# Optimization experiments

Measured on AMD Instinct MI355X. Metric: run time of the kernel, lower is better.

## Reference

```python
import jax, jax.numpy as jnp
import numpy as np

N = 100000
E = 3200000
F_IN = 16
H = 128
LAT = 64
L = 3
G = 1024


def setup_inputs() -> dict:
    key = jax.random.key(0)
    ks = jax.random.split(key, 12)
    x = jax.random.normal(ks[0], (N, F_IN), dtype=jnp.float32)
    edge_index = jax.random.randint(ks[1], (2, E), 0, N, dtype=jnp.int64)
    batch = jnp.sort(jax.random.randint(ks[2], (N,), 0, G, dtype=jnp.int64))
    batch = batch.at[-1].set(G - 1)  # ensure batch.max()+1 == G
    s_in = 1.0 / np.sqrt(F_IN)
    s_h = 1.0 / np.sqrt(H)
    W_in = jax.random.uniform(ks[3], (F_IN, H), jnp.float32, -s_in, s_in)
    b_in = jax.random.uniform(ks[4], (H,), jnp.float32, -s_in, s_in)
    W_msg = jax.random.uniform(ks[5], (L, H, H), jnp.float32, -s_h, s_h)
    b_msg = jax.random.uniform(ks[6], (L, H), jnp.float32, -s_h, s_h)
    W_mean = jax.random.uniform(ks[7], (H, LAT), jnp.float32, -s_h, s_h)
    b_mean = jax.random.uniform(ks[8], (LAT,), jnp.float32, -s_h, s_h)
    W_logvar = jax.random.uniform(ks[9], (H, LAT), jnp.float32, -s_h, s_h)
    b_logvar = jax.random.uniform(ks[10], (LAT,), jnp.float32, -s_h, s_h)
    return {
        "x": x, "edge_index": edge_index, "batch": batch, "num_graphs": G,
        "W_in": W_in, "b_in": b_in, "W_msg": W_msg, "b_msg": b_msg,
        "W_mean": W_mean, "b_mean": b_mean,
        "W_logvar": W_logvar, "b_logvar": b_logvar,
    }


def reference(x, edge_index, batch, num_graphs, W_in, b_in, W_msg, b_msg,
              W_mean, b_mean, W_logvar, b_logvar):
    src, dst = edge_index[0], edge_index[1]
    n = x.shape[0]
    # input net: Linear + ReLU
    h = jax.nn.relu(x @ W_in + b_in)  # [N, H]
    # stacked message-passing: transform, gather at src, scatter-add to dst, ReLU
    for l in range(L):
        m = h @ W_msg[l] + b_msg[l]                    # [N, H]
        agg = jax.ops.segment_sum(m[src], dst, num_segments=n)  # [N, H]
        h = jax.nn.relu(agg)
    # graph-level sum pooling via index_add over batch ids
    graph_embedding = jax.ops.segment_sum(h, batch, num_segments=num_graphs)  # [G, H]
    z_mean = graph_embedding @ W_mean + b_mean
    z_logvar = graph_embedding @ W_logvar + b_logvar
    return (z_mean, z_logvar)
```

## Files before the change

kernel.cpp:

```cpp
#include <hip/hip_runtime.h>

constexpr int N_  = 100000;
constexpr int E_  = 3200000;
constexpr int FIN = 16;
constexpr int H_  = 128;
constexpr int LAT = 64;
constexpr int L_  = 3;
constexpr int G_  = 1024;

constexpr int BSH = 9;
constexpr int BNODES = 1 << BSH;
constexpr int NB_ = (N_ + BNODES - 1) / BNODES;
constexpr int FILL_NB = 512;
constexpr int FILL_CHUNK = E_ / FILL_NB;

using bf16x8 = __attribute__((ext_vector_type(8))) short;
using f32x4  = __attribute__((ext_vector_type(4))) float;

__device__ inline float bflo(unsigned int u) {
  union { unsigned int i; float f; } v; v.i = u << 16; return v.f;
}
__device__ inline float bfhi(unsigned int u) {
  union { unsigned int i; float f; } v; v.i = u & 0xffff0000u; return v.f;
}
__device__ inline unsigned short f2bf(float f) {
  union { float f; unsigned int i; } v; v.f = f;
  unsigned int r = v.i + 0x7fffu + ((v.i >> 16) & 1u);
  return (unsigned short)(r >> 16);
}

__global__ __launch_bounds__(256) void k_wconv(const float* __restrict__ W,
                                               unsigned short* __restrict__ Wt,
                                               int* __restrict__ bcnt) {
  if (blockIdx.x == 0) {
    for (int i = threadIdx.x; i < NB_; i += 256) bcnt[i] = 0;
  }
  const int idx = blockIdx.x * 256 + threadIdx.x;
  if (idx < L_ * H_ * H_) {
    const int l = idx >> 14, rem = idx & 16383;
    const int c = rem >> 7, k = rem & 127;
    Wt[idx] = f2bf(W[l * H_ * H_ + k * H_ + c]);
  }
}

__global__ __launch_bounds__(256) void k_input(const float* __restrict__ x,
                                               const float* __restrict__ Win,
                                               const float* __restrict__ bin,
                                               unsigned short* __restrict__ h) {
  __shared__ float Wl[FIN * H_];
  __shared__ float xl[4 * FIN];
  const int tid = threadIdx.x;
  for (int i = tid; i < FIN * H_; i += 256) Wl[i] = Win[i];
  const int n0 = blockIdx.x * 4;
  if (tid < 4 * FIN) xl[tid] = x[(size_t)n0 * FIN + tid];
  __syncthreads();
  const int nl = tid >> 6, l = tid & 63;
  float a0 = bin[2 * l], a1 = bin[2 * l + 1];
#pragma unroll
  for (int k = 0; k < FIN; ++k) {
    const float xv = xl[nl * FIN + k];
    a0 += xv * Wl[k * H_ + 2 * l];
    a1 += xv * Wl[k * H_ + 2 * l + 1];
  }
  const unsigned int packed =
      (unsigned int)f2bf(fmaxf(a0, 0.f)) | ((unsigned int)f2bf(fmaxf(a1, 0.f)) << 16);
  *reinterpret_cast<unsigned int*>(h + (size_t)(n0 + nl) * H_ + 2 * l) = packed;
}

__global__ __launch_bounds__(256) void k_msg_mfma(const unsigned short* __restrict__ h,
                                                  const unsigned short* __restrict__ Wt,
                                                  const float* __restrict__ b,
                                                  unsigned short* __restrict__ m) {
  __shared__ unsigned short st[4][32][40];
  const int wave = threadIdx.x >> 6;
  const int lane = threadIdx.x & 63;
  const int r = lane & 15;
  const int g = lane >> 4;
  const int n0 = blockIdx.x * 32;
  const int cb = wave * 32;

  f32x4 acc[2][2] = {};
#pragma unroll
  for (int kk = 0; kk < 4; ++kk) {
    const int koff = kk * 32 + g * 8;
    const bf16x8 a0 = *reinterpret_cast<const bf16x8*>(h + (size_t)(n0 + r) * H_ + koff);
    const bf16x8 a1 = *reinterpret_cast<const bf16x8*>(h + (size_t)(n0 + 16 + r) * H_ + koff);
    const bf16x8 b0 = *reinterpret_cast<const bf16x8*>(Wt + (size_t)(cb + r) * H_ + koff);
    const bf16x8 b1 = *reinterpret_cast<const bf16x8*>(Wt + (size_t)(cb + 16 + r) * H_ + koff);
    acc[0][0] = __builtin_amdgcn_mfma_f32_16x16x32_bf16(a0, b0, acc[0][0], 0, 0, 0);
    acc[0][1] = __builtin_amdgcn_mfma_f32_16x16x32_bf16(a0, b1, acc[0][1], 0, 0, 0);
    acc[1][0] = __builtin_amdgcn_mfma_f32_16x16x32_bf16(a1, b0, acc[1][0], 0, 0, 0);
    acc[1][1] = __builtin_amdgcn_mfma_f32_16x16x32_bf16(a1, b1, acc[1][1], 0, 0, 0);
  }

  const float bc0 = b[cb + r];
  const float bc1 = b[cb + 16 + r];
#pragma unroll
  for (int rt = 0; rt < 2; ++rt)
#pragma unroll
    for (int ct = 0; ct < 2; ++ct) {
      const float bc = ct ? bc1 : bc0;
#pragma unroll
      for (int j = 0; j < 4; ++j)
        st[wave][rt * 16 + g * 4 + j][ct * 16 + r] = f2bf(acc[rt][ct][j] + bc);
    }
  __syncthreads();
#pragma unroll
  for (int p = 0; p < 2; ++p) {
    const int lr = p * 16 + (lane >> 2);
    const int seg = lane & 3;
    const bf16x8 v = *reinterpret_cast<const bf16x8*>(&st[wave][lr][seg * 8]);
    *reinterpret_cast<bf16x8*>(m + (size_t)(n0 + lr) * H_ + cb + seg * 8) = v;
  }
}

__global__ __launch_bounds__(256) void k_bhist(const int* __restrict__ ei,
                                               int* __restrict__ bcnt) {
  __shared__ int lh[NB_];
  for (int i = threadIdx.x; i < NB_; i += 256) lh[i] = 0;
  __syncthreads();
  const int gid = blockIdx.x * 256 + threadIdx.x;
  const int stride = gridDim.x * 256;
  for (int e = gid; e < E_; e += stride) atomicAdd(&lh[ei[E_ + e] >> BSH], 1);
  __syncthreads();
  for (int i = threadIdx.x; i < NB_; i += 256)
    if (lh[i]) atomicAdd(&bcnt[i], lh[i]);
}

__global__ __launch_bounds__(256) void k_bscan(const int* __restrict__ bcnt,
                                               int* __restrict__ boff,
                                               int* __restrict__ bcur,
                                               float* __restrict__ ge) {
  __shared__ int s[256];
  const int t = threadIdx.x;
  s[t] = (t < NB_) ? bcnt[t] : 0;
  __syncthreads();
  for (int off = 1; off < 256; off <<= 1) {
    const int add = (t >= off) ? s[t - off] : 0;
    __syncthreads();
    s[t] += add;
    __syncthreads();
  }
  const int ex = (t == 0) ? 0 : s[t - 1];
  if (t < NB_) { boff[t] = ex; bcur[t] = ex; }
  if (t == 0) boff[NB_] = s[NB_ - 1];
  float4 z = make_float4(0.f, 0.f, 0.f, 0.f);
  float4* g4 = reinterpret_cast<float4*>(ge);
  for (int i = t; i < G_ * H_ / 4; i += 256) g4[i] = z;
}

__global__ __launch_bounds__(256) void k_bfill(const int* __restrict__ ei,
                                               int* __restrict__ bcur,
                                               unsigned int* __restrict__ ebuf) {
  __shared__ int lh[NB_], lbase[NB_];
  const int t = threadIdx.x;
  for (int i = t; i < NB_; i += 256) lh[i] = 0;
  __syncthreads();
  const int e0 = blockIdx.x * FILL_CHUNK;
  const int e1 = e0 + FILL_CHUNK;
  for (int e = e0 + t; e < e1; e += 256) atomicAdd(&lh[ei[E_ + e] >> BSH], 1);
  __syncthreads();
  for (int i = t; i < NB_; i += 256) {
    const int c = lh[i];
    lbase[i] = c ? atomicAdd(&bcur[i], c) : 0;
  }
  __syncthreads();
  for (int i = t; i < NB_; i += 256) lh[i] = 0;
  __syncthreads();
  for (int e = e0 + t; e < e1; e += 256) {
    const int src = ei[e], dst = ei[E_ + e];
    const int b = dst >> BSH;
    const int pos = lbase[b] + atomicAdd(&lh[b], 1);
    ebuf[pos] = ((unsigned)src << BSH) | (unsigned)(dst & (BNODES - 1));
  }
}

__global__ __launch_bounds__(256) void k_bcsr(const unsigned int* __restrict__ ebuf,
                                              const int* __restrict__ boff,
                                              int* __restrict__ rowp,
                                              int* __restrict__ ssrc) {
  __shared__ int sdeg[BNODES];
  __shared__ int scur[BNODES];
  __shared__ int part[256];
  const int b = blockIdx.x;
  const int nbase = b << BSH;
  const int ncnt = min(BNODES, N_ - nbase);
  const int ebeg = boff[b], eend = boff[b + 1];
  const int t = threadIdx.x;
  for (int i = t; i < BNODES; i += 256) { sdeg[i] = 0; scur[i] = 0; }
  __syncthreads();
  for (int e = ebeg + t; e < eend; e += 256)
    atomicAdd(&sdeg[ebuf[e] & (BNODES - 1)], 1);
  __syncthreads();
  const int i0 = 2 * t, i1 = 2 * t + 1;
  const int d0 = sdeg[i0];
  part[t] = d0 + sdeg[i1];
  __syncthreads();
  for (int off = 1; off < 256; off <<= 1) {
    const int add = (t >= off) ? part[t - off] : 0;
    __syncthreads();
    part[t] += add;
    __syncthreads();
  }
  const int ex = (t == 0) ? 0 : part[t - 1];
  sdeg[i0] = ex;
  sdeg[i1] = ex + d0;
  __syncthreads();
  for (int i = t; i < ncnt; i += 256) rowp[nbase + i] = ebeg + sdeg[i];
  if (b == NB_ - 1 && t == 0) rowp[N_] = E_;
  for (int e = ebeg + t; e < eend; e += 256) {
    const unsigned int ed = ebuf[e];
    const int ld = ed & (BNODES - 1);
    const int pos = ebeg + sdeg[ld] + atomicAdd(&scur[ld], 1);
    ssrc[pos] = (int)(ed >> BSH);
  }
}

__global__ __launch_bounds__(256) void k_gather(const unsigned short* __restrict__ m,
                                                const int* __restrict__ rowptr,
                                                const int* __restrict__ ssrc,
                                                unsigned short* __restrict__ h) {
  const int n = blockIdx.x * 4 + (threadIdx.x >> 6);
  const int c2 = threadIdx.x & 63;
  const int beg = rowptr[n], end = rowptr[n + 1];
  const unsigned short* mc = m + 2 * c2;
  float a0 = 0.f, a1 = 0.f;
  int i = beg;
  for (; i + 15 < end; i += 16) {
    int s[16];
#pragma unroll
    for (int u = 0; u < 16; ++u) s[u] = ssrc[i + u];
    unsigned int v[16];
#pragma unroll
    for (int u = 0; u < 16; ++u)
      v[u] = *reinterpret_cast<const unsigned int*>(mc + (size_t)s[u] * H_);
#pragma unroll
    for (int u = 0; u < 16; ++u) { a0 += bflo(v[u]); a1 += bfhi(v[u]); }
  }
  for (; i + 3 < end; i += 4) {
    int s[4];
#pragma unroll
    for (int u = 0; u < 4; ++u) s[u] = ssrc[i + u];
    unsigned int v[4];
#pragma unroll
    for (int u = 0; u < 4; ++u)
      v[u] = *reinterpret_cast<const unsigned int*>(mc + (size_t)s[u] * H_);
#pragma unroll
    for (int u = 0; u < 4; ++u) { a0 += bflo(v[u]); a1 += bfhi(v[u]); }
  }
  for (; i < end; ++i) {
    const unsigned int v = *reinterpret_cast<const unsigned int*>(mc + (size_t)ssrc[i] * H_);
    a0 += bflo(v);  a1 += bfhi(v);
  }
  const unsigned int packed =
      (unsigned int)f2bf(fmaxf(a0, 0.f)) | ((unsigned int)f2bf(fmaxf(a1, 0.f)) << 16);
  *reinterpret_cast<unsigned int*>(h + (size_t)n * H_ + 2 * c2) = packed;
}

constexpr int POOL_CHUNK = 128;
__global__ __launch_bounds__(128) void k_pool(const unsigned short* __restrict__ h,
                                              const int* __restrict__ batch,
                                              float* __restrict__ ge) {
  __shared__ int bl[POOL_CHUNK];
  const int tid = threadIdx.x;
  const int start = blockIdx.x * POOL_CHUNK;
  const int cnt = min(POOL_CHUNK, N_ - start);
  if (tid < cnt) bl[tid] = batch[start + tid];
  __syncthreads();
  float run = 0.f;
  int cur = bl[0];
  for (int i = 0; i < cnt; ++i) {
    const int bid = bl[i];
    const float v = bflo((unsigned int)h[(size_t)(start + i) * H_ + tid]);
    if (bid != cur) {
      unsafeAtomicAdd(&ge[(size_t)cur * H_ + tid], run);
      run = 0.f;
      cur = bid;
    }
    run += v;
  }
  unsafeAtomicAdd(&ge[(size_t)cur * H_ + tid], run);
}

__global__ __launch_bounds__(128) void k_out(const float* __restrict__ ge,
                                             const float* __restrict__ Wm,
                                             const float* __restrict__ bm,
                                             const float* __restrict__ Wv,
                                             const float* __restrict__ bv,
                                             float* __restrict__ out) {
  __shared__ float gl[H_];
  const int g = blockIdx.x, tid = threadIdx.x;
  gl[tid] = ge[(size_t)g * H_ + tid];
  __syncthreads();
  const bool is_mean = (tid < LAT);
  const float* W = is_mean ? Wm : Wv;
  const float* bb = is_mean ? bm : bv;
  const int c = tid & 63;
  float acc = bb[c];
#pragma unroll 8
  for (int k = 0; k < H_; ++k) acc += gl[k] * W[k * LAT + c];
  const size_t off = is_mean ? 0 : (size_t)G_ * LAT;
  out[off + (size_t)g * LAT + c] = acc;
}

extern "C" void kernel_launch(void* const* d_in, const int* in_sizes, int n_in,
                              void* d_out, int out_size, void* d_ws, size_t ws_size,
                              hipStream_t stream) {
  const float* x     = (const float*)d_in[0];
  const int*   ei    = (const int*)d_in[1];
  const int*   batch = (const int*)d_in[2];
  const float* Win   = (const float*)d_in[4];
  const float* bin   = (const float*)d_in[5];
  const float* Wmsg  = (const float*)d_in[6];
  const float* bmsg  = (const float*)d_in[7];
  const float* Wmean = (const float*)d_in[8];
  const float* bmean = (const float*)d_in[9];
  const float* Wlv   = (const float*)d_in[10];
  const float* blv   = (const float*)d_in[11];
  float* out = (float*)d_out;

  char* p = (char*)d_ws;
  unsigned short* h  = (unsigned short*)p;  p += (size_t)N_ * H_ * 2;
  unsigned short* m  = (unsigned short*)p;  p += (size_t)N_ * H_ * 2;
  unsigned int* ebuf = (unsigned int*)p;    p += (size_t)E_ * 4;
  int* ssrc          = (int*)p;             p += (size_t)E_ * 4;
  int* rowp          = (int*)p;             p += (size_t)(N_ + 1) * 4;
  unsigned short* Wt = (unsigned short*)p;  p += (size_t)L_ * H_ * H_ * 2;
  float* ge          = (float*)p;           p += (size_t)G_ * H_ * 4;
  int* bcnt          = (int*)p;             p += (size_t)NB_ * 4;
  int* boff          = (int*)p;             p += (size_t)(NB_ + 1) * 4;
  int* bcur          = (int*)p;             p += (size_t)NB_ * 4;

  k_wconv<<<(L_ * H_ * H_ + 255) / 256, 256, 0, stream>>>(Wmsg, Wt, bcnt);

  k_bhist<<<256, 256, 0, stream>>>(ei, bcnt);
  k_bscan<<<1, 256, 0, stream>>>(bcnt, boff, bcur, ge);
  k_bfill<<<FILL_NB, 256, 0, stream>>>(ei, bcur, ebuf);
  k_bcsr<<<NB_, 256, 0, stream>>>(ebuf, boff, rowp, ssrc);

  k_input<<<N_ / 4, 256, 0, stream>>>(x, Win, bin, h);

  for (int l = 0; l < L_; ++l) {
    k_msg_mfma<<<N_ / 32, 256, 0, stream>>>(h, Wt + (size_t)l * H_ * H_,
                                            bmsg + (size_t)l * H_, m);
    k_gather<<<N_ / 4, 256, 0, stream>>>(m, rowp, ssrc, h);
  }

  k_pool<<<(N_ + POOL_CHUNK - 1) / POOL_CHUNK, 128, 0, stream>>>(h, batch, ge);

  k_out<<<G_, 128, 0, stream>>>(ge, Wmean, bmean, Wlv, blv, out);
}
```

Baseline: 559.3 us.

## Fuse gather with next layer's MFMA transform and merge weight-convert with input layer

Adds a k_gm kernel that gathers and sums neighbour messages for 32 nodes into shared memory, applies ReLU, then runs the next layer's bf16 MFMA transform directly. This removes the h write and re-read between the gather and the message kernels for layers two and three. The weight conversion and the input Linear+ReLU are merged into one launch, and the bucket-histogram grid is doubled. The fused gather runs only 256 threads per 32 nodes, so it has less parallelism for latency hiding, and it needs a second message buffer.

```diff
diff --git a/kernel.cpp b/kernel.cpp
--- a/kernel.cpp
+++ b/kernel.cpp
@@ -14,6 +14,8 @@
 constexpr int FILL_NB = 512;
 constexpr int FILL_CHUNK = E_ / FILL_NB;
 
+constexpr int WCONV_BLOCKS = (L_ * H_ * H_) / 256;
+
 using bf16x8 = __attribute__((ext_vector_type(8))) short;
 using f32x4  = __attribute__((ext_vector_type(4))) float;
 
@@ -29,29 +31,27 @@
   return (unsigned short)(r >> 16);
 }
 
-__global__ __launch_bounds__(256) void k_wconv(const float* __restrict__ W,
+__global__ __launch_bounds__(256) void k_winit(const float* __restrict__ W,
                                                unsigned short* __restrict__ Wt,
-                                               int* __restrict__ bcnt) {
-  if (blockIdx.x == 0) {
-    for (int i = threadIdx.x; i < NB_; i += 256) bcnt[i] = 0;
-  }
-  const int idx = blockIdx.x * 256 + threadIdx.x;
-  if (idx < L_ * H_ * H_) {
+                                               int* __restrict__ bcnt,
+                                               const float* __restrict__ x,
+                                               const float* __restrict__ Win,
+                                               const float* __restrict__ bin,
+                                               unsigned short* __restrict__ h) {
+  const int tid = threadIdx.x;
+  if (blockIdx.x < WCONV_BLOCKS) {
+    if (blockIdx.x == 0)
+      for (int i = tid; i < NB_; i += 256) bcnt[i] = 0;
+    const int idx = blockIdx.x * 256 + tid;
     const int l = idx >> 14, rem = idx & 16383;
     const int c = rem >> 7, k = rem & 127;
     Wt[idx] = f2bf(W[l * H_ * H_ + k * H_ + c]);
-  }
-}
-
-__global__ __launch_bounds__(256) void k_input(const float* __restrict__ x,
-                                               const float* __restrict__ Win,
-                                               const float* __restrict__ bin,
-                                               unsigned short* __restrict__ h) {
+    return;
+  }
   __shared__ float Wl[FIN * H_];
   __shared__ float xl[4 * FIN];
-  const int tid = threadIdx.x;
   for (int i = tid; i < FIN * H_; i += 256) Wl[i] = Win[i];
-  const int n0 = blockIdx.x * 4;
+  const int n0 = (blockIdx.x - WCONV_BLOCKS) * 4;
   if (tid < 4 * FIN) xl[tid] = x[(size_t)n0 * FIN + tid];
   __syncthreads();
   const int nl = tid >> 6, l = tid & 63;
@@ -111,6 +111,95 @@
     const int seg = lane & 3;
     const bf16x8 v = *reinterpret_cast<const bf16x8*>(&st[wave][lr][seg * 8]);
     *reinterpret_cast<bf16x8*>(m + (size_t)(n0 + lr) * H_ + cb + seg * 8) = v;
+  }
+}
+
+__global__ __launch_bounds__(256) void k_gm(const unsigned short* __restrict__ m_in,
+                                            const int* __restrict__ rowptr,
+                                            const int* __restrict__ ssrc,
+                                            const unsigned short* __restrict__ Wt,
+                                            const float* __restrict__ b,
+                                            unsigned short* __restrict__ m_out) {
+  __shared__ unsigned int hl[32][68];
+  __shared__ unsigned short st[4][32][40];
+  const int wave = threadIdx.x >> 6;
+  const int lane = threadIdx.x & 63;
+  const int n0 = blockIdx.x * 32;
+  const unsigned short* mc = m_in + 2 * lane;
+
+  for (int j = 0; j < 8; ++j) {
+    const int row = wave * 8 + j;
+    const int n = n0 + row;
+    const int beg = rowptr[n], end = rowptr[n + 1];
+    float a0 = 0.f, a1 = 0.f;
+    int i = beg;
+    for (; i + 15 < end; i += 16) {
+      int s[16];
+#pragma unroll
+      for (int u = 0; u < 16; ++u) s[u] = ssrc[i + u];
+      unsigned int v[16];
+#pragma unroll
+      for (int u = 0; u < 16; ++u)
+        v[u] = *reinterpret_cast<const unsigned int*>(mc + (size_t)s[u] * H_);
+#pragma unroll
+      for (int u = 0; u < 16; ++u) { a0 += bflo(v[u]); a1 += bfhi(v[u]); }
+    }
+    for (; i + 3 < end; i += 4) {
+      int s[4];
+#pragma unroll
+      for (int u = 0; u < 4; ++u) s[u] = ssrc[i + u];
+      unsigned int v[4];
+#pragma unroll
+      for (int u = 0; u < 4; ++u)
+        v[u] = *reinterpret_cast<const unsigned int*>(mc + (size_t)s[u] * H_);
+#pragma unroll
+      for (int u = 0; u < 4; ++u) { a0 += bflo(v[u]); a1 += bfhi(v[u]); }
+    }
+    for (; i < end; ++i) {
+      const unsigned int v = *reinterpret_cast<const unsigned int*>(mc + (size_t)ssrc[i] * H_);
+      a0 += bflo(v);  a1 += bfhi(v);
+    }
+    hl[row][lane] =
+        (unsigned int)f2bf(fmaxf(a0, 0.f)) | ((unsigned int)f2bf(fmaxf(a1, 0.f)) << 16);
+  }
+  __syncthreads();
+
+  const int r = lane & 15;
+  const int g = lane >> 4;
+  const int cb = wave * 32;
+  f32x4 acc[2][2] = {};
+#pragma unroll
+  for (int kk = 0; kk < 4; ++kk) {
+    const int koff  = kk * 32 + g * 8;
+    const int koffu = kk * 16 + g * 4;
+    const bf16x8 a0 = *reinterpret_cast<const bf16x8*>(&hl[r][koffu]);
+    const bf16x8 a1 = *reinterpret_cast<const bf16x8*>(&hl[16 + r][koffu]);
+    const bf16x8 b0 = *reinterpret_cast<const bf16x8*>(Wt + (size_t)(cb + r) * H_ + koff);
+    const bf16x8 b1 = *reinterpret_cast<const bf16x8*>(Wt + (size_t)(cb + 16 + r) * H_ + koff);
+    acc[0][0] = __builtin_amdgcn_mfma_f32_16x16x32_bf16(a0, b0, acc[0][0], 0, 0, 0);
+    acc[0][1] = __builtin_amdgcn_mfma_f32_16x16x32_bf16(a0, b1, acc[0][1], 0, 0, 0);
+    acc[1][0] = __builtin_amdgcn_mfma_f32_16x16x32_bf16(a1, b0, acc[1][0], 0, 0, 0);
+    acc[1][1] = __builtin_amdgcn_mfma_f32_16x16x32_bf16(a1, b1, acc[1][1], 0, 0, 0);
+  }
+
+  const float bc0 = b[cb + r];
+  const float bc1 = b[cb + 16 + r];
+#pragma unroll
+  for (int rt = 0; rt < 2; ++rt)
+#pragma unroll
+    for (int ct = 0; ct < 2; ++ct) {
+      const float bc = ct ? bc1 : bc0;
+#pragma unroll
+      for (int j = 0; j < 4; ++j)
+        st[wave][rt * 16 + g * 4 + j][ct * 16 + r] = f2bf(acc[rt][ct][j] + bc);
+    }
+  __syncthreads();
+#pragma unroll
+  for (int p = 0; p < 2; ++p) {
+    const int lr = p * 16 + (lane >> 2);
+    const int seg = lane & 3;
+    const bf16x8 v = *reinterpret_cast<const bf16x8*>(&st[wave][lr][seg * 8]);
+    *reinterpret_cast<bf16x8*>(m_out + (size_t)(n0 + lr) * H_ + cb + seg * 8) = v;
   }
 }
 
@@ -321,7 +410,8 @@
 
   char* p = (char*)d_ws;
   unsigned short* h  = (unsigned short*)p;  p += (size_t)N_ * H_ * 2;
-  unsigned short* m  = (unsigned short*)p;  p += (size_t)N_ * H_ * 2;
+  unsigned short* mA = (unsigned short*)p;  p += (size_t)N_ * H_ * 2;
+  unsigned short* mB = (unsigned short*)p;  p += (size_t)N_ * H_ * 2;
   unsigned int* ebuf = (unsigned int*)p;    p += (size_t)E_ * 4;
   int* ssrc          = (int*)p;             p += (size_t)E_ * 4;
   int* rowp          = (int*)p;             p += (size_t)(N_ + 1) * 4;
@@ -331,22 +421,20 @@
   int* boff          = (int*)p;             p += (size_t)(NB_ + 1) * 4;
   int* bcur          = (int*)p;             p += (size_t)NB_ * 4;
 
-  k_wconv<<<(L_ * H_ * H_ + 255) / 256, 256, 0, stream>>>(Wmsg, Wt, bcnt);
-
-  k_bhist<<<256, 256, 0, stream>>>(ei, bcnt);
+  k_winit<<<WCONV_BLOCKS + N_ / 4, 256, 0, stream>>>(Wmsg, Wt, bcnt, x, Win, bin, h);
+
+  k_bhist<<<512, 256, 0, stream>>>(ei, bcnt);
   k_bscan<<<1, 256, 0, stream>>>(bcnt, boff, bcur, ge);
   k_bfill<<<FILL_NB, 256, 0, stream>>>(ei, bcur, ebuf);
   k_bcsr<<<NB_, 256, 0, stream>>>(ebuf, boff, rowp, ssrc);
 
-  k_input<<<N_ / 4, 256, 0, stream>>>(x, Win, bin, h);
-
-  for (int l = 0; l < L_; ++l) {
-    k_msg_mfma<<<N_ / 32, 256, 0, stream>>>(h, Wt + (size_t)l * H_ * H_,
-                                            bmsg + (size_t)l * H_, m);
-    k_gather<<<N_ / 4, 256, 0, stream>>>(m, rowp, ssrc, h);
-  }
+  k_msg_mfma<<<N_ / 32, 256, 0, stream>>>(h, Wt, bmsg, mA);
+  k_gm<<<N_ / 32, 256, 0, stream>>>(mA, rowp, ssrc,
+                                    Wt + (size_t)H_ * H_, bmsg + H_, mB);
+  k_gm<<<N_ / 32, 256, 0, stream>>>(mB, rowp, ssrc,
+                                    Wt + (size_t)2 * H_ * H_, bmsg + 2 * H_, mA);
+  k_gather<<<N_ / 4, 256, 0, stream>>>(mA, rowp, ssrc, h);
 
   k_pool<<<(N_ + POOL_CHUNK - 1) / POOL_CHUNK, 128, 0, stream>>>(h, batch, ge);
-
   k_out<<<G_, 128, 0, stream>>>(ge, Wmean, bmean, Wlv, blv, out);
 }
```

After: 559.0 us. Within noise of the previous version (-0.1%).

## Chunk message features into 16-column slabs and gather per chunk with wave-split edges

Applied to the files above, without the earlier changes.

Stores messages and hidden states in a chunked layout of 8 slabs of 16 bf16 columns (N×16 each), so each gather block works on one 32-byte column slab whose 3.2 MB working set is more likely to stay in cache during random source reads. The gather kernel now spreads a node's edges across 16 lane groups with a shuffle reduction, and uses a fixed grid of persistent slots. Weight conversion and the input layer are merged into one launch, and the histogram grid is doubled. In exchange, each node's edge list and row pointers are read eight times, once per slab, and the pool kernel reads with a 32-byte stride.

```diff
diff --git a/kernel.cpp b/kernel.cpp
--- a/kernel.cpp
+++ b/kernel.cpp
@@ -14,6 +14,9 @@
 constexpr int FILL_NB = 512;
 constexpr int FILL_CHUNK = E_ / FILL_NB;
 
+constexpr int WCONV_BLOCKS = (L_ * H_ * H_) / 256;
+constexpr int GSLOTS = 4096;
+
 using bf16x8 = __attribute__((ext_vector_type(8))) short;
 using f32x4  = __attribute__((ext_vector_type(4))) float;
 
@@ -29,29 +32,27 @@
   return (unsigned short)(r >> 16);
 }
 
-__global__ __launch_bounds__(256) void k_wconv(const float* __restrict__ W,
+__global__ __launch_bounds__(256) void k_winit(const float* __restrict__ W,
                                                unsigned short* __restrict__ Wt,
-                                               int* __restrict__ bcnt) {
-  if (blockIdx.x == 0) {
-    for (int i = threadIdx.x; i < NB_; i += 256) bcnt[i] = 0;
-  }
-  const int idx = blockIdx.x * 256 + threadIdx.x;
-  if (idx < L_ * H_ * H_) {
+                                               int* __restrict__ bcnt,
+                                               const float* __restrict__ x,
+                                               const float* __restrict__ Win,
+                                               const float* __restrict__ bin,
+                                               unsigned short* __restrict__ h) {
+  const int tid = threadIdx.x;
+  if (blockIdx.x < WCONV_BLOCKS) {
+    if (blockIdx.x == 0)
+      for (int i = tid; i < NB_; i += 256) bcnt[i] = 0;
+    const int idx = blockIdx.x * 256 + tid;
     const int l = idx >> 14, rem = idx & 16383;
     const int c = rem >> 7, k = rem & 127;
     Wt[idx] = f2bf(W[l * H_ * H_ + k * H_ + c]);
-  }
-}
-
-__global__ __launch_bounds__(256) void k_input(const float* __restrict__ x,
-                                               const float* __restrict__ Win,
-                                               const float* __restrict__ bin,
-                                               unsigned short* __restrict__ h) {
+    return;
+  }
   __shared__ float Wl[FIN * H_];
   __shared__ float xl[4 * FIN];
-  const int tid = threadIdx.x;
   for (int i = tid; i < FIN * H_; i += 256) Wl[i] = Win[i];
-  const int n0 = blockIdx.x * 4;
+  const int n0 = (blockIdx.x - WCONV_BLOCKS) * 4;
   if (tid < 4 * FIN) xl[tid] = x[(size_t)n0 * FIN + tid];
   __syncthreads();
   const int nl = tid >> 6, l = tid & 63;
@@ -67,10 +68,11 @@
   *reinterpret_cast<unsigned int*>(h + (size_t)(n0 + nl) * H_ + 2 * l) = packed;
 }
 
-__global__ __launch_bounds__(256) void k_msg_mfma(const unsigned short* __restrict__ h,
+template <int CHUNKED>
+__global__ __launch_bounds__(256) void k_msg_mfma(const unsigned short* __restrict__ A,
                                                   const unsigned short* __restrict__ Wt,
                                                   const float* __restrict__ b,
-                                                  unsigned short* __restrict__ m) {
+                                                  unsigned short* __restrict__ m8) {
   __shared__ unsigned short st[4][32][40];
   const int wave = threadIdx.x >> 6;
   const int lane = threadIdx.x & 63;
@@ -83,8 +85,15 @@
 #pragma unroll
   for (int kk = 0; kk < 4; ++kk) {
     const int koff = kk * 32 + g * 8;
-    const bf16x8 a0 = *reinterpret_cast<const bf16x8*>(h + (size_t)(n0 + r) * H_ + koff);
-    const bf16x8 a1 = *reinterpret_cast<const bf16x8*>(h + (size_t)(n0 + 16 + r) * H_ + koff);
+    bf16x8 a0, a1;
+    if (CHUNKED) {
+      const size_t cbase = (size_t)(2 * kk + (g >> 1)) * N_ * 16 + (g & 1) * 8;
+      a0 = *reinterpret_cast<const bf16x8*>(A + cbase + (size_t)(n0 + r) * 16);
+      a1 = *reinterpret_cast<const bf16x8*>(A + cbase + (size_t)(n0 + 16 + r) * 16);
+    } else {
+      a0 = *reinterpret_cast<const bf16x8*>(A + (size_t)(n0 + r) * H_ + koff);
+      a1 = *reinterpret_cast<const bf16x8*>(A + (size_t)(n0 + 16 + r) * H_ + koff);
+    }
     const bf16x8 b0 = *reinterpret_cast<const bf16x8*>(Wt + (size_t)(cb + r) * H_ + koff);
     const bf16x8 b1 = *reinterpret_cast<const bf16x8*>(Wt + (size_t)(cb + 16 + r) * H_ + koff);
     acc[0][0] = __builtin_amdgcn_mfma_f32_16x16x32_bf16(a0, b0, acc[0][0], 0, 0, 0);
@@ -110,7 +119,8 @@
     const int lr = p * 16 + (lane >> 2);
     const int seg = lane & 3;
     const bf16x8 v = *reinterpret_cast<const bf16x8*>(&st[wave][lr][seg * 8]);
-    *reinterpret_cast<bf16x8*>(m + (size_t)(n0 + lr) * H_ + cb + seg * 8) = v;
+    *reinterpret_cast<bf16x8*>(m8 + (size_t)(2 * wave + (seg >> 1)) * N_ * 16 +
+                               (size_t)(n0 + lr) * 16 + (seg & 1) * 8) = v;
   }
 }
 
@@ -216,49 +226,54 @@
   }
 }
 
-__global__ __launch_bounds__(256) void k_gather(const unsigned short* __restrict__ m,
-                                                const int* __restrict__ rowptr,
-                                                const int* __restrict__ ssrc,
-                                                unsigned short* __restrict__ h) {
-  const int n = blockIdx.x * 4 + (threadIdx.x >> 6);
-  const int c2 = threadIdx.x & 63;
-  const int beg = rowptr[n], end = rowptr[n + 1];
-  const unsigned short* mc = m + 2 * c2;
-  float a0 = 0.f, a1 = 0.f;
-  int i = beg;
-  for (; i + 15 < end; i += 16) {
-    int s[16];
-#pragma unroll
-    for (int u = 0; u < 16; ++u) s[u] = ssrc[i + u];
-    unsigned int v[16];
-#pragma unroll
-    for (int u = 0; u < 16; ++u)
-      v[u] = *reinterpret_cast<const unsigned int*>(mc + (size_t)s[u] * H_);
-#pragma unroll
-    for (int u = 0; u < 16; ++u) { a0 += bflo(v[u]); a1 += bfhi(v[u]); }
-  }
-  for (; i + 3 < end; i += 4) {
-    int s[4];
-#pragma unroll
-    for (int u = 0; u < 4; ++u) s[u] = ssrc[i + u];
-    unsigned int v[4];
-#pragma unroll
-    for (int u = 0; u < 4; ++u)
-      v[u] = *reinterpret_cast<const unsigned int*>(mc + (size_t)s[u] * H_);
-#pragma unroll
-    for (int u = 0; u < 4; ++u) { a0 += bflo(v[u]); a1 += bfhi(v[u]); }
-  }
-  for (; i < end; ++i) {
-    const unsigned int v = *reinterpret_cast<const unsigned int*>(mc + (size_t)ssrc[i] * H_);
-    a0 += bflo(v);  a1 += bfhi(v);
-  }
-  const unsigned int packed =
-      (unsigned int)f2bf(fmaxf(a0, 0.f)) | ((unsigned int)f2bf(fmaxf(a1, 0.f)) << 16);
-  *reinterpret_cast<unsigned int*>(h + (size_t)n * H_ + 2 * c2) = packed;
+__global__ __launch_bounds__(256) void k_gather8(const unsigned short* __restrict__ m8,
+                                                 const int* __restrict__ rowptr,
+                                                 const int* __restrict__ ssrc,
+                                                 unsigned short* __restrict__ h8) {
+  const int chunk = blockIdx.x & 7;
+  const int lane = threadIdx.x & 63;
+  const int wave = threadIdx.x >> 6;
+  const int slot = (blockIdx.x >> 3) * 4 + wave;
+  const int eg = lane >> 2;
+  const int cl = lane & 3;
+  const unsigned short* mc = m8 + (size_t)chunk * N_ * 16 + cl * 4;
+  unsigned short* hc = h8 + (size_t)chunk * N_ * 16;
+
+  for (int n = slot; n < N_; n += GSLOTS) {
+    const int beg = rowptr[n], end = rowptr[n + 1];
+    float a0 = 0.f, a1 = 0.f, a2 = 0.f, a3 = 0.f;
+    int i = beg + eg;
+    for (; i + 16 < end; i += 32) {
+      const int s0 = ssrc[i];
+      const int s1 = ssrc[i + 16];
+      const uint2 v0 = *reinterpret_cast<const uint2*>(mc + (size_t)s0 * 16);
+      const uint2 v1 = *reinterpret_cast<const uint2*>(mc + (size_t)s1 * 16);
+      a0 += bflo(v0.x);  a1 += bfhi(v0.x);  a2 += bflo(v0.y);  a3 += bfhi(v0.y);
+      a0 += bflo(v1.x);  a1 += bfhi(v1.x);  a2 += bflo(v1.y);  a3 += bfhi(v1.y);
+    }
+    if (i < end) {
+      const int s = ssrc[i];
+      const uint2 v = *reinterpret_cast<const uint2*>(mc + (size_t)s * 16);
+      a0 += bflo(v.x);  a1 += bfhi(v.x);  a2 += bflo(v.y);  a3 += bfhi(v.y);
+    }
+#pragma unroll
+    for (int mask = 4; mask <= 32; mask <<= 1) {
+      a0 += __shfl_xor(a0, mask);
+      a1 += __shfl_xor(a1, mask);
+      a2 += __shfl_xor(a2, mask);
+      a3 += __shfl_xor(a3, mask);
+    }
+    if (lane < 4) {
+      uint2 o;
+      o.x = (unsigned int)f2bf(fmaxf(a0, 0.f)) | ((unsigned int)f2bf(fmaxf(a1, 0.f)) << 16);
+      o.y = (unsigned int)f2bf(fmaxf(a2, 0.f)) | ((unsigned int)f2bf(fmaxf(a3, 0.f)) << 16);
+      *reinterpret_cast<uint2*>(hc + (size_t)n * 16 + cl * 4) = o;
+    }
+  }
 }
 
 constexpr int POOL_CHUNK = 128;
-__global__ __launch_bounds__(128) void k_pool(const unsigned short* __restrict__ h,
+__global__ __launch_bounds__(128) void k_pool(const unsigned short* __restrict__ h8,
                                               const int* __restrict__ batch,
                                               float* __restrict__ ge) {
   __shared__ int bl[POOL_CHUNK];
@@ -267,11 +282,12 @@
   const int cnt = min(POOL_CHUNK, N_ - start);
   if (tid < cnt) bl[tid] = batch[start + tid];
   __syncthreads();
+  const unsigned short* hc = h8 + (size_t)(tid >> 4) * N_ * 16 + (tid & 15);
   float run = 0.f;
   int cur = bl[0];
   for (int i = 0; i < cnt; ++i) {
     const int bid = bl[i];
-    const float v = bflo((unsigned int)h[(size_t)(start + i) * H_ + tid]);
+    const float v = bflo((unsigned int)hc[(size_t)(start + i) * 16]);
     if (bid != cur) {
       unsafeAtomicAdd(&ge[(size_t)cur * H_ + tid], run);
       run = 0.f;
@@ -321,7 +337,8 @@
 
   char* p = (char*)d_ws;
   unsigned short* h  = (unsigned short*)p;  p += (size_t)N_ * H_ * 2;
-  unsigned short* m  = (unsigned short*)p;  p += (size_t)N_ * H_ * 2;
+  unsigned short* mA = (unsigned short*)p;  p += (size_t)N_ * H_ * 2;
+  unsigned short* mB = (unsigned short*)p;  p += (size_t)N_ * H_ * 2;
   unsigned int* ebuf = (unsigned int*)p;    p += (size_t)E_ * 4;
   int* ssrc          = (int*)p;             p += (size_t)E_ * 4;
   int* rowp          = (int*)p;             p += (size_t)(N_ + 1) * 4;
@@ -331,22 +348,22 @@
   int* boff          = (int*)p;             p += (size_t)(NB_ + 1) * 4;
   int* bcur          = (int*)p;             p += (size_t)NB_ * 4;
 
-  k_wconv<<<(L_ * H_ * H_ + 255) / 256, 256, 0, stream>>>(Wmsg, Wt, bcnt);
-
-  k_bhist<<<256, 256, 0, stream>>>(ei, bcnt);
+  k_winit<<<WCONV_BLOCKS + N_ / 4, 256, 0, stream>>>(Wmsg, Wt, bcnt, x, Win, bin, h);
+
+  k_bhist<<<512, 256, 0, stream>>>(ei, bcnt);
   k_bscan<<<1, 256, 0, stream>>>(bcnt, boff, bcur, ge);
   k_bfill<<<FILL_NB, 256, 0, stream>>>(ei, bcur, ebuf);
   k_bcsr<<<NB_, 256, 0, stream>>>(ebuf, boff, rowp, ssrc);
 
-  k_input<<<N_ / 4, 256, 0, stream>>>(x, Win, bin, h);
-
-  for (int l = 0; l < L_; ++l) {
-    k_msg_mfma<<<N_ / 32, 256, 0, stream>>>(h, Wt + (size_t)l * H_ * H_,
-                                            bmsg + (size_t)l * H_, m);
-    k_gather<<<N_ / 4, 256, 0, stream>>>(m, rowp, ssrc, h);
-  }
+  k_msg_mfma<0><<<N_ / 32, 256, 0, stream>>>(h, Wt, bmsg, mA);
+  k_gather8<<<GSLOTS * 2, 256, 0, stream>>>(mA, rowp, ssrc, h);
+  k_msg_mfma<1><<<N_ / 32, 256, 0, stream>>>(h, Wt + (size_t)H_ * H_,
+                                             bmsg + H_, mB);
+  k_gather8<<<GSLOTS * 2, 256, 0, stream>>>(mB, rowp, ssrc, h);
+  k_msg_mfma<1><<<N_ / 32, 256, 0, stream>>>(h, Wt + (size_t)2 * H_ * H_,
+                                             bmsg + 2 * H_, mA);
+  k_gather8<<<GSLOTS * 2, 256, 0, stream>>>(mA, rowp, ssrc, h);
 
   k_pool<<<(N_ + POOL_CHUNK - 1) / POOL_CHUNK, 128, 0, stream>>>(h, batch, ge);
-
   k_out<<<G_, 128, 0, stream>>>(ge, Wmean, bmean, Wlv, blv, out);
 }
```

New measurement: 815.3 us. +45.8%, slower.

## Sort CSR neighbors by source bucket and fuse weight conversion with input layer

Applied to the files above, without the earlier changes.

The per-block CSR build now counts edges by (destination node, source bucket of 4096 nodes) and prefix-scans those keys, so each node's neighbor list comes out grouped by source range. This is meant to improve cache locality of the gather kernel's row reads in all three layers. The weight conversion and input linear layer are merged into one launch to save a kernel, and the histogram grid is doubled. The larger shared-memory key array (512x25 ints) and the serial per-thread scan add cost to the CSR build and may reduce its occupancy.

```diff
diff --git a/kernel.cpp b/kernel.cpp
--- a/kernel.cpp
+++ b/kernel.cpp
@@ -14,6 +14,12 @@
 constexpr int FILL_NB = 512;
 constexpr int FILL_CHUNK = E_ / FILL_NB;
 
+constexpr int SRCB_SHIFT = 12;
+constexpr int NSRCB = (N_ + (1 << SRCB_SHIFT) - 1) >> SRCB_SHIFT;
+constexpr int NKEYS = BNODES * NSRCB;
+
+constexpr int WCONV_BLOCKS = (L_ * H_ * H_) / 256;
+
 using bf16x8 = __attribute__((ext_vector_type(8))) short;
 using f32x4  = __attribute__((ext_vector_type(4))) float;
 
@@ -29,29 +35,27 @@
   return (unsigned short)(r >> 16);
 }
 
-__global__ __launch_bounds__(256) void k_wconv(const float* __restrict__ W,
+__global__ __launch_bounds__(256) void k_winit(const float* __restrict__ W,
                                                unsigned short* __restrict__ Wt,
-                                               int* __restrict__ bcnt) {
-  if (blockIdx.x == 0) {
-    for (int i = threadIdx.x; i < NB_; i += 256) bcnt[i] = 0;
-  }
-  const int idx = blockIdx.x * 256 + threadIdx.x;
-  if (idx < L_ * H_ * H_) {
+                                               int* __restrict__ bcnt,
+                                               const float* __restrict__ x,
+                                               const float* __restrict__ Win,
+                                               const float* __restrict__ bin,
+                                               unsigned short* __restrict__ h) {
+  const int tid = threadIdx.x;
+  if (blockIdx.x < WCONV_BLOCKS) {
+    if (blockIdx.x == 0)
+      for (int i = tid; i < NB_; i += 256) bcnt[i] = 0;
+    const int idx = blockIdx.x * 256 + tid;
     const int l = idx >> 14, rem = idx & 16383;
     const int c = rem >> 7, k = rem & 127;
     Wt[idx] = f2bf(W[l * H_ * H_ + k * H_ + c]);
-  }
-}
-
-__global__ __launch_bounds__(256) void k_input(const float* __restrict__ x,
-                                               const float* __restrict__ Win,
-                                               const float* __restrict__ bin,
-                                               unsigned short* __restrict__ h) {
+    return;
+  }
   __shared__ float Wl[FIN * H_];
   __shared__ float xl[4 * FIN];
-  const int tid = threadIdx.x;
   for (int i = tid; i < FIN * H_; i += 256) Wl[i] = Win[i];
-  const int n0 = blockIdx.x * 4;
+  const int n0 = (blockIdx.x - WCONV_BLOCKS) * 4;
   if (tid < 4 * FIN) xl[tid] = x[(size_t)n0 * FIN + tid];
   __syncthreads();
   const int nl = tid >> 6, l = tid & 63;
@@ -179,22 +183,29 @@
                                               const int* __restrict__ boff,
                                               int* __restrict__ rowp,
                                               int* __restrict__ ssrc) {
-  __shared__ int sdeg[BNODES];
-  __shared__ int scur[BNODES];
+  __shared__ int sdeg[NKEYS];
   __shared__ int part[256];
   const int b = blockIdx.x;
   const int nbase = b << BSH;
   const int ncnt = min(BNODES, N_ - nbase);
   const int ebeg = boff[b], eend = boff[b + 1];
   const int t = threadIdx.x;
-  for (int i = t; i < BNODES; i += 256) { sdeg[i] = 0; scur[i] = 0; }
-  __syncthreads();
-  for (int e = ebeg + t; e < eend; e += 256)
-    atomicAdd(&sdeg[ebuf[e] & (BNODES - 1)], 1);
-  __syncthreads();
-  const int i0 = 2 * t, i1 = 2 * t + 1;
-  const int d0 = sdeg[i0];
-  part[t] = d0 + sdeg[i1];
+  for (int i = t; i < NKEYS; i += 256) sdeg[i] = 0;
+  __syncthreads();
+  for (int e = ebeg + t; e < eend; e += 256) {
+    const unsigned int ed = ebuf[e];
+    const int key = (int)(ed & (BNODES - 1)) * NSRCB + (int)(ed >> (BSH + SRCB_SHIFT));
+    atomicAdd(&sdeg[key], 1);
+  }
+  __syncthreads();
+  constexpr int KPT = NKEYS / 256;
+  {
+    int s = 0;
+    const int k0 = t * KPT;
+#pragma unroll 10
+    for (int k = 0; k < KPT; ++k) s += sdeg[k0 + k];
+    part[t] = s;
+  }
   __syncthreads();
   for (int off = 1; off < 256; off <<= 1) {
     const int add = (t >= off) ? part[t - off] : 0;
@@ -202,16 +213,24 @@
     part[t] += add;
     __syncthreads();
   }
-  const int ex = (t == 0) ? 0 : part[t - 1];
-  sdeg[i0] = ex;
-  sdeg[i1] = ex + d0;
-  __syncthreads();
-  for (int i = t; i < ncnt; i += 256) rowp[nbase + i] = ebeg + sdeg[i];
+  {
+    int run = (t == 0) ? 0 : part[t - 1];
+    const int k0 = t * KPT;
+#pragma unroll 10
+    for (int k = 0; k < KPT; ++k) {
+      const int c = sdeg[k0 + k];
+      sdeg[k0 + k] = run;
+      run += c;
+    }
+  }
+  __syncthreads();
+  for (int i = t; i < ncnt; i += 256) rowp[nbase + i] = ebeg + sdeg[i * NSRCB];
   if (b == NB_ - 1 && t == 0) rowp[N_] = E_;
+  __syncthreads();
   for (int e = ebeg + t; e < eend; e += 256) {
     const unsigned int ed = ebuf[e];
-    const int ld = ed & (BNODES - 1);
-    const int pos = ebeg + sdeg[ld] + atomicAdd(&scur[ld], 1);
+    const int key = (int)(ed & (BNODES - 1)) * NSRCB + (int)(ed >> (BSH + SRCB_SHIFT));
+    const int pos = ebeg + atomicAdd(&sdeg[key], 1);
     ssrc[pos] = (int)(ed >> BSH);
   }
 }
@@ -331,14 +350,12 @@
   int* boff          = (int*)p;             p += (size_t)(NB_ + 1) * 4;
   int* bcur          = (int*)p;             p += (size_t)NB_ * 4;
 
-  k_wconv<<<(L_ * H_ * H_ + 255) / 256, 256, 0, stream>>>(Wmsg, Wt, bcnt);
-
-  k_bhist<<<256, 256, 0, stream>>>(ei, bcnt);
+  k_winit<<<WCONV_BLOCKS + N_ / 4, 256, 0, stream>>>(Wmsg, Wt, bcnt, x, Win, bin, h);
+
+  k_bhist<<<512, 256, 0, stream>>>(ei, bcnt);
   k_bscan<<<1, 256, 0, stream>>>(bcnt, boff, bcur, ge);
   k_bfill<<<FILL_NB, 256, 0, stream>>>(ei, bcur, ebuf);
   k_bcsr<<<NB_, 256, 0, stream>>>(ebuf, boff, rowp, ssrc);
-
-  k_input<<<N_ / 4, 256, 0, stream>>>(x, Win, bin, h);
 
   for (int l = 0; l < L_; ++l) {
     k_msg_mfma<<<N_ / 32, 256, 0, stream>>>(h, Wt + (size_t)l * H_ * H_,
@@ -347,6 +364,5 @@
   }
 
   k_pool<<<(N_ + POOL_CHUNK - 1) / POOL_CHUNK, 128, 0, stream>>>(h, batch, ge);
-
   k_out<<<G_, 128, 0, stream>>>(ge, Wmean, bmean, Wlv, blv, out);
 }
```

New measurement: 564.0 us. Within noise of the previous version (+0.8%).
